# Optimization experiments

Hardware: AMD Instinct MI355X
Metric: run time of the kernel (lower is better)

## Reference

```python
import jax, jax.numpy as jnp
import numpy as np

B, L, HID = 8, 1025, 1024
H, KV, DH = 16, 4, 64
EPS = 1e-6
ROPE_BASE = 10000.0


def _rms_norm(x, w):
    var = jnp.mean(jnp.square(x), axis=-1, keepdims=True)
    return x * jax.lax.rsqrt(var + EPS) * w


def _rotate_half(x):
    x1, x2 = jnp.split(x, 2, axis=-1)
    return jnp.concatenate([-x2, x1], axis=-1)


def _rope_cache(seq_len, dim):
    inv_freq = 1.0 / (ROPE_BASE ** (jnp.arange(0, dim, 2, dtype=jnp.float32) / dim))
    pos = jnp.arange(seq_len, dtype=jnp.float32)
    freqs = pos[:, None] * inv_freq[None, :]            # [L_img, dim/2]
    emb = jnp.concatenate([freqs, freqs], axis=-1)       # [L_img, dim]
    return jnp.cos(emb), jnp.sin(emb)


def setup_inputs() -> dict:
    key = jax.random.key(0)
    ks = jax.random.split(key, 5)
    s_in = 1.0
    s_q = float(np.sqrt(2.0 / (HID + H * DH)))
    s_kv = float(np.sqrt(2.0 / (HID + KV * DH)))
    s_o = float(np.sqrt(2.0 / (H * DH + HID)) / np.sqrt(2.0))
    return {
        "inputs": jax.random.normal(ks[0], (B, L, HID), jnp.float32) * s_in,
        "Wq": jax.random.normal(ks[1], (H * DH, HID), jnp.float32) * s_q,
        "Wk": jax.random.normal(ks[2], (KV * DH, HID), jnp.float32) * s_kv,
        "Wv": jax.random.normal(ks[3], (KV * DH, HID), jnp.float32) * s_kv,
        "Wo": jax.random.normal(ks[4], (HID, H * DH), jnp.float32) * s_o,
        "q_norm_w": jnp.ones((DH,), jnp.float32),
        "k_norm_w": jnp.ones((DH,), jnp.float32),
    }


def reference(inputs, Wq, Wk, Wv, Wo, q_norm_w, k_norm_w):
    b, l, _ = inputs.shape
    # projections (torch Linear: x @ W.T), reshape to heads, QK RMSNorm
    q = (inputs @ Wq.T).reshape(b, l, H, DH)
    k = (inputs @ Wk.T).reshape(b, l, KV, DH)
    v = (inputs @ Wv.T).reshape(b, l, KV, DH)
    q = _rms_norm(q, q_norm_w).transpose(0, 2, 1, 3)    # [B,H,L,DH]
    k = _rms_norm(k, k_norm_w).transpose(0, 2, 1, 3)    # [B,KV,L,DH]
    v = v.transpose(0, 2, 1, 3)                          # [B,KV,L,DH]

    # RoPE only on image tokens (skip first action token)
    l_img = l - 1
    cos, sin = _rope_cache(l_img, DH)                    # [L_img, DH]
    cos = cos[None, None].astype(q.dtype)
    sin = sin[None, None].astype(q.dtype)
    q_img = q[:, :, 1:]
    k_img = k[:, :, 1:]
    q = jnp.concatenate([q[:, :, :1], q_img * cos + _rotate_half(q_img) * sin], axis=2)
    k = jnp.concatenate([k[:, :, :1], k_img * cos + _rotate_half(k_img) * sin], axis=2)

    # GQA: repeat kv heads
    rep = H // KV
    k = jnp.repeat(k, rep, axis=1)                       # [B,H,L,DH]
    v = jnp.repeat(v, rep, axis=1)

    # manual attention: NOTE no 1/sqrt(DH) scaling (faithful to source)
    scores = jnp.einsum("bhqd,bhkd->bhqk", q, k)
    attn = jax.nn.softmax(scores.astype(jnp.float32), axis=-1).astype(q.dtype)
    out = jnp.einsum("bhqk,bhkd->bhqd", attn, v)         # [B,H,L,DH]
    out = out.transpose(0, 2, 1, 3).reshape(b, l, H * DH)
    return out @ Wo.T
```

## Files before the change

kernel.cpp:

```cpp
#include <hip/hip_runtime.h>
#include <hip/hip_bf16.h>

using bf16 = __hip_bfloat16;
typedef __bf16 bf16x8 __attribute__((ext_vector_type(8)));
typedef float f32x4 __attribute__((ext_vector_type(4)));
typedef short short8 __attribute__((ext_vector_type(8)));
typedef unsigned short ushort4v __attribute__((ext_vector_type(4)));

#define MFMA16(a, b, c) __builtin_amdgcn_mfma_f32_16x16x32_bf16((a), (b), (c), 0, 0, 0)

constexpr int B_ = 8, L_ = 1025, H_ = 16, KV_ = 4;
constexpr int LKP_ = 1088;
constexpr int M_ = B_ * L_;

constexpr int NX = 8396800, NWQ = 1048576, NWK = 262144, NWV = 262144,
              NWO = 1048576, NNW = 64;

__device__ __forceinline__ void gl_lds16(const bf16* g, bf16* l) {
  __builtin_amdgcn_global_load_lds(
      (const __attribute__((address_space(1))) void*)g,
      (__attribute__((address_space(3))) void*)l, 16, 0, 0);
}

template <int NWG>
__device__ __forceinline__ int xcd_swz(int orig) {
  constexpr int q = NWG >> 3, r = NWG & 7;
  const int x = orig & 7, idx = orig >> 3;
  return (x < r ? x * (q + 1) : r * (q + 1) + (x - r) * q) + idx;
}

__global__ __launch_bounds__(64) void detect_dtype(const unsigned short* qw_raw,
                                                   int* flag) {
  if (threadIdx.x == 0) flag[0] = (qw_raw[0] == 0x3F80) ? 0 : 1;
}

__global__ __launch_bounds__(256) void convert_all(
    const void* s0, const void* s1, const void* s2, const void* s3,
    const void* s4, const void* s5, const void* s6,
    bf16* d0, bf16* d1, bf16* d2, bf16* d3, bf16* d4, bf16* d5, bf16* d6,
    const int* flag) {
  const int f = *flag;
  const int tid = blockIdx.x * blockDim.x + threadIdx.x;
  const int stride = gridDim.x * blockDim.x;
  auto conv = [&](const void* s, bf16* d, int n) {
    const int n8 = n >> 3;
    if (f) {
      const f32x4* sf = (const f32x4*)s;
      short8* dd = (short8*)d;
      for (int i = tid; i < n8; i += stride) {
        const f32x4 v0 = sf[2 * i], v1 = sf[2 * i + 1];
        short8 o;
#pragma unroll
        for (int j = 0; j < 4; ++j) {
          o[j]     = __builtin_bit_cast(short, __float2bfloat16(v0[j]));
          o[j + 4] = __builtin_bit_cast(short, __float2bfloat16(v1[j]));
        }
        dd[i] = o;
      }
    } else {
      const short8* su = (const short8*)s;
      short8* dd = (short8*)d;
      for (int i = tid; i < n8; i += stride) dd[i] = su[i];
    }
  };
  conv(s0, d0, NX);
  conv(s1, d1, NWQ);
  conv(s2, d2, NWK);
  conv(s3, d3, NWV);
  conv(s4, d4, NWO);
  conv(s5, d5, NNW);
  conv(s6, d6, NNW);
}

__global__ __launch_bounds__(256) void zero_pads(bf16* Kb, bf16* VT) {
  const int idx = blockIdx.x * 256 + threadIdx.x;
  const bf16 z = __float2bfloat16(0.f);
  {
    const int g = idx / 4032, rem = idx % 4032;
    const int r = rem >> 6, d = rem & 63;
    Kb[((size_t)g * LKP_ + 1025 + r) * 64 + d] = z;
  }
  {
    const int row = idx / 63, c = idx % 63;
    VT[(size_t)row * LKP_ + 1025 + c] = z;
  }
}

template <int EPI, int NT, int NWG>
__global__ __launch_bounds__(256) void gemm_bt(
    const bf16* __restrict__ X, const bf16* __restrict__ W0,
    const bf16* __restrict__ W1, const bf16* __restrict__ W2,
    void* __restrict__ O0, bf16* __restrict__ O1, bf16* __restrict__ O2,
    const bf16* __restrict__ qw, const bf16* __restrict__ kw,
    const int* flag) {
  const int wg = xcd_swz<NWG>(blockIdx.x);
  const int m0 = (wg / NT) * 128;
  const int n0 = (wg % NT) * 128;

  int outf32 = 0;
  if constexpr (EPI == 0) outf32 = *flag;

  const bf16* W;
  int nw0;
  if constexpr (EPI == 0) {
    W = W0; nw0 = n0;
  } else {
    if (n0 < 1024)      { W = W0; nw0 = n0; }
    else if (n0 < 1280) { W = W1; nw0 = n0 - 1024; }
    else                { W = W2; nw0 = n0 - 1280; }
  }

  __shared__ bf16 As[128 * 64];
  __shared__ bf16 Bs[128 * 64];

  const int tid = threadIdx.x;
  const int lane = tid & 63, wid = tid >> 6;
  const int wr = wid >> 1, wc = wid & 1;
  const int lo = lane & 15, g = lane >> 4;

  const f32x4 zero4 = {0.f, 0.f, 0.f, 0.f};
  f32x4 acc[4][4];
#pragma unroll
  for (int i = 0; i < 4; ++i)
#pragma unroll
    for (int j = 0; j < 4; ++j) acc[i][j] = zero4;

  const int rr = tid >> 3;
  const int csw = ((tid & 7) ^ (rr & 7)) * 8;
  const bf16* xp[4];
  const bf16* wp[4];
#pragma unroll
  for (int is = 0; is < 4; ++is) {
    int rx = m0 + rr + 32 * is;
    if (rx > M_ - 1) rx = M_ - 1;
    xp[is] = X + (size_t)rx * 1024 + csw;
    wp[is] = W + (size_t)(nw0 + rr + 32 * is) * 1024 + csw;
  }

  for (int kt = 0; kt < 16; ++kt) {
#pragma unroll
    for (int is = 0; is < 4; ++is) {
      gl_lds16(xp[is], &As[is * 2048 + (size_t)tid * 8]);
      gl_lds16(wp[is], &Bs[is * 2048 + (size_t)tid * 8]);
      xp[is] += 64; wp[is] += 64;
    }
    __syncthreads();

    bf16x8 a[2][4], bb[2][4];
#pragma unroll
    for (int kk = 0; kk < 2; ++kk) {
      const int sw = ((4 * kk + g) ^ (lo & 7)) * 8;
#pragma unroll
      for (int i = 0; i < 4; ++i)
        a[kk][i] = *reinterpret_cast<const bf16x8*>(&As[(wr * 64 + i * 16 + lo) * 64 + sw]);
#pragma unroll
      for (int j = 0; j < 4; ++j)
        bb[kk][j] = *reinterpret_cast<const bf16x8*>(&Bs[(wc * 64 + j * 16 + lo) * 64 + sw]);
    }
#pragma unroll
    for (int kk = 0; kk < 2; ++kk)
#pragma unroll
      for (int i = 0; i < 4; ++i)
#pragma unroll
        for (int j = 0; j < 4; ++j)
          acc[i][j] = MFMA16(a[kk][i], bb[kk][j], acc[i][j]);
    __syncthreads();
  }

  const bool qkreg = (EPI == 1) && (n0 < 1280);
  float wv[4];
  float invf0 = 0.f, invf1 = 0.f;
  if (qkreg) {
    const bf16* w = (n0 < 1024) ? qw : kw;
#pragma unroll
    for (int j = 0; j < 4; ++j) wv[j] = __bfloat162float(w[j * 16 + lo]);
    constexpr float c = -0.41524101186092029f;
    invf0 = exp2f((float)lo * c);
    invf1 = invf0 * exp2f(16.f * c);
  }

#pragma unroll
  for (int i = 0; i < 4; ++i) {
#pragma unroll
    for (int ii = 0; ii < 4; ++ii) {
      const int m = m0 + wr * 64 + i * 16 + g * 4 + ii;
      if (m >= M_) continue;
      const int b = m / L_;
      const int l = m % L_;
      float fv[4];
#pragma unroll
      for (int j = 0; j < 4; ++j) fv[j] = acc[i][j][ii];

      if (qkreg) {
#pragma unroll
        for (int j = 0; j < 4; ++j)
          fv[j] = __bfloat162float(__float2bfloat16(fv[j]));
        float ss = fv[0] * fv[0] + fv[1] * fv[1] + fv[2] * fv[2] + fv[3] * fv[3];
        ss += __shfl_xor(ss, 1);
        ss += __shfl_xor(ss, 2);
        ss += __shfl_xor(ss, 4);
        ss += __shfl_xor(ss, 8);
        const float r = rsqrtf(ss * (1.f / 64.f) + 1e-6f);
#pragma unroll
        for (int j = 0; j < 4; ++j) fv[j] *= r * wv[j];
        if (l > 0) {
          const float pos = (float)(l - 1);
          float sn0, cs0, sn1, cs1;
          __sincosf(pos * invf0, &sn0, &cs0);
          __sincosf(pos * invf1, &sn1, &cs1);
          const float a0 = fv[0], a2 = fv[2];
          fv[0] = a0 * cs0 - a2 * sn0;
          fv[2] = a2 * cs0 + a0 * sn0;
          const float a1 = fv[1], a3 = fv[3];
          fv[1] = a1 * cs1 - a3 * sn1;
          fv[3] = a3 * cs1 + a1 * sn1;
        }
      }

#pragma unroll
      for (int j = 0; j < 4; ++j) {
        const int n = n0 + wc * 64 + j * 16 + lo;
        const float f = fv[j];
        if constexpr (EPI == 0) {
          if (outf32) ((float*)O0)[(size_t)m * 1024 + n] = f;
          else        ((bf16*)O0)[(size_t)m * 1024 + n] = __float2bfloat16(f);
        } else {
          const bf16 v = __float2bfloat16(f);
          if (n < 1024) {
            ((bf16*)O0)[((size_t)(b * H_ + (n >> 6)) * L_ + l) * 64 + (n & 63)] = v;
          } else if (n < 1280) {
            const int c2 = n - 1024;
            O1[((size_t)(b * KV_ + (c2 >> 6)) * LKP_ + l) * 64 + (c2 & 63)] = v;
          } else {
            const int c2 = n - 1280;
            O2[((size_t)(b * KV_ + (c2 >> 6)) * 64 + (c2 & 63)) * LKP_ + l] = v;
          }
        }
      }
    }
  }
}

__global__ __launch_bounds__(512) void attn(
    const bf16* __restrict__ Q, const bf16* __restrict__ Kt,
    const bf16* __restrict__ VT, bf16* __restrict__ AO) {
  const int tid = threadIdx.x, lane = tid & 63, w = tid >> 6;
  const int lo = lane & 15, g = lane >> 4;
  const int qt = blockIdx.x, h = blockIdx.y, b = blockIdx.z;
  const int kv = h >> 2;

  __shared__ unsigned short Ks[64 * 64];
  __shared__ unsigned short Vs[64 * 64];
  __shared__ unsigned short Ps[8 * 16 * 64];

  const bf16* qbase = Q + (size_t)(b * H_ + h) * L_ * 64;
  int qrow = qt * 128 + w * 16 + lo;
  if (qrow > L_ - 1) qrow = L_ - 1;
  const bf16x8 qf0 = *reinterpret_cast<const bf16x8*>(qbase + (size_t)qrow * 64 + g * 8);
  const bf16x8 qf1 = *reinterpret_cast<const bf16x8*>(qbase + (size_t)qrow * 64 + 32 + g * 8);

  const f32x4 zero4 = {0.f, 0.f, 0.f, 0.f};
  f32x4 o[4];
  float mi = -3e38f, li = 0.f;
#pragma unroll
  for (int i = 0; i < 4; ++i) o[i] = zero4;

  const int sr = tid >> 3;
  const int scol = (tid & 7) * 8;
  const int swcol = ((tid & 7) ^ (sr & 7)) * 8;
  const bf16* kbase = Kt + ((size_t)(b * KV_ + kv) * LKP_ + sr) * 64 + scol;
  const bf16* vbase = VT + ((size_t)(b * KV_ + kv) * 64 + sr) * LKP_ + scol;

  const int sw0 = (g ^ (lo & 7)) * 8;
  const int sw1 = ((4 | g) ^ (lo & 7)) * 8;
  const int pswa = ((g >> 1) ^ (lo & 7));

  for (int kt = 0; kt < 17; ++kt) {
    const int k0 = kt * 64;
    const short8 ka = *reinterpret_cast<const short8*>(kbase + (size_t)k0 * 64);
    const short8 va = *reinterpret_cast<const short8*>(vbase + k0);
    __syncthreads();
    *reinterpret_cast<short8*>(&Ks[sr * 64 + swcol]) = ka;
    *reinterpret_cast<short8*>(&Vs[sr * 64 + swcol]) = va;
    __syncthreads();

    f32x4 s[4];
#pragma unroll
    for (int kb = 0; kb < 4; ++kb) {
      f32x4 t = zero4;
      const bf16x8 ka0 = *reinterpret_cast<const bf16x8*>(&Ks[(kb * 16 + lo) * 64 + sw0]);
      const bf16x8 ka1 = *reinterpret_cast<const bf16x8*>(&Ks[(kb * 16 + lo) * 64 + sw1]);
      t = MFMA16(ka0, qf0, t);
      t = MFMA16(ka1, qf1, t);
      s[kb] = t;
    }
    if (kt == 16) {
#pragma unroll
      for (int kb = 0; kb < 4; ++kb)
#pragma unroll
        for (int i = 0; i < 4; ++i)
          if (k0 + kb * 16 + g * 4 + i >= L_) s[kb][i] = -1e30f;
    }

    float t0 = fmaxf(fmaxf(s[0][0], s[0][1]), fmaxf(s[0][2], s[0][3]));
    float t1 = fmaxf(fmaxf(s[1][0], s[1][1]), fmaxf(s[1][2], s[1][3]));
    float t2 = fmaxf(fmaxf(s[2][0], s[2][1]), fmaxf(s[2][2], s[2][3]));
    float t3 = fmaxf(fmaxf(s[3][0], s[3][1]), fmaxf(s[3][2], s[3][3]));
    float tm = fmaxf(fmaxf(t0, t1), fmaxf(t2, t3));
    tm = fmaxf(tm, __shfl_xor(tm, 16));
    tm = fmaxf(tm, __shfl_xor(tm, 32));
    if (!__all(tm <= mi)) {
      const float mn = fmaxf(mi, tm);
      const float sc = __expf(mi - mn);
      mi = mn;
      li *= sc;
#pragma unroll
      for (int db = 0; db < 4; ++db)
#pragma unroll
        for (int i = 0; i < 4; ++i) o[db][i] *= sc;
    }
#pragma unroll
    for (int kb = 0; kb < 4; ++kb)
#pragma unroll
      for (int i = 0; i < 4; ++i) s[kb][i] = __expf(s[kb][i] - mi);
    float p0 = (s[0][0] + s[0][1]) + (s[0][2] + s[0][3]);
    float p1 = (s[1][0] + s[1][1]) + (s[1][2] + s[1][3]);
    float p2 = (s[2][0] + s[2][1]) + (s[2][2] + s[2][3]);
    float p3 = (s[3][0] + s[3][1]) + (s[3][2] + s[3][3]);
    float ps = (p0 + p1) + (p2 + p3);
    ps += __shfl_xor(ps, 16);
    ps += __shfl_xor(ps, 32);
    li += ps;

#pragma unroll
    for (int kb = 0; kb < 4; ++kb) {
      ushort4v pk;
#pragma unroll
      for (int i = 0; i < 4; ++i)
        pk[i] = __builtin_bit_cast(unsigned short, __float2bfloat16(s[kb][i]));
      *reinterpret_cast<ushort4v*>(
          &Ps[w * 1024 + lo * 64 + ((2 * kb) ^ pswa ^ (g >> 1) ^ (g >> 1)) * 8 +
              (((2 * kb + (g >> 1)) ^ (lo & 7)) - ((2 * kb) ^ pswa ^ (g >> 1) ^ (g >> 1))) * 8 +
              (g & 1) * 4]) = pk;
    }

    const bf16x8 pb0 = *reinterpret_cast<const bf16x8*>(&Ps[w * 1024 + lo * 64 + sw0]);
    const bf16x8 pb1 = *reinterpret_cast<const bf16x8*>(&Ps[w * 1024 + lo * 64 + sw1]);
#pragma unroll
    for (int db = 0; db < 4; ++db) {
      const bf16x8 va0 = *reinterpret_cast<const bf16x8*>(&Vs[(db * 16 + lo) * 64 + sw0]);
      const bf16x8 va1 = *reinterpret_cast<const bf16x8*>(&Vs[(db * 16 + lo) * 64 + sw1]);
      o[db] = MFMA16(va0, pb0, o[db]);
      o[db] = MFMA16(va1, pb1, o[db]);
    }
  }

  const int qr = qt * 128 + w * 16 + lo;
  if (qr < L_) {
    const float inv = 1.f / li;
    unsigned* base = (unsigned*)(AO + ((size_t)b * L_ + qr) * 1024 + h * 64);
#pragma unroll
    for (int db = 0; db < 4; ++db) {
#pragma unroll
      for (int i2 = 0; i2 < 4; i2 += 2) {
        const unsigned u0 = __builtin_bit_cast(unsigned short,
                                __float2bfloat16(o[db][i2] * inv));
        const unsigned u1 = __builtin_bit_cast(unsigned short,
                                __float2bfloat16(o[db][i2 + 1] * inv));
        base[(db * 16 + 4 * g + i2) >> 1] = u0 | (u1 << 16);
      }
    }
  }
}

extern "C" void kernel_launch(void* const* d_in, const int* in_sizes, int n_in,
                              void* d_out, int out_size, void* d_ws, size_t ws_size,
                              hipStream_t stream) {
  (void)in_sizes; (void)n_in; (void)out_size; (void)ws_size;

  char* wsb = (char*)d_ws;
  int* flagp = (int*)wsb;
  bf16* cX  = (bf16*)(wsb + 16);
  bf16* cWq = cX + NX;
  bf16* cWk = cWq + NWQ;
  bf16* cWv = cWk + NWK;
  bf16* cWo = cWv + NWV;
  bf16* cqw = cWo + NWO;
  bf16* ckw = cqw + NNW;
  bf16* Qb  = ckw + NNW;
  bf16* Kb  = Qb  + (size_t)B_ * H_ * L_ * 64;
  bf16* VTb = Kb  + (size_t)B_ * KV_ * LKP_ * 64;
  bf16* AOb = VTb + (size_t)B_ * KV_ * 64 * LKP_;

  detect_dtype<<<1, 64, 0, stream>>>((const unsigned short*)d_in[5], flagp);
  convert_all<<<2048, 256, 0, stream>>>(
      d_in[0], d_in[1], d_in[2], d_in[3], d_in[4], d_in[5], d_in[6],
      cX, cWq, cWk, cWv, cWo, cqw, ckw, flagp);
  zero_pads<<<504, 256, 0, stream>>>(Kb, VTb);

  gemm_bt<1, 12, 780><<<780, 256, 0, stream>>>(cX, cWq, cWk, cWv, Qb, Kb, VTb,
                                               cqw, ckw, nullptr);
  attn<<<dim3(9, 16, 8), 512, 0, stream>>>(Qb, Kb, VTb, AOb);
  gemm_bt<0, 8, 520><<<520, 256, 0, stream>>>(AOb, cWo, nullptr, nullptr, d_out,
                                              nullptr, nullptr, nullptr, nullptr,
                                              flagp);
}
```

Measured before the change: 212.8 us.

## Double-buffer GEMM LDS tiles and prefetch K/V tiles in attention loop

The projection GEMM now uses two 128x32 LDS buffers per operand with a K-step of 32. The next tile's global-to-LDS loads are issued before computing on the current one, so load latency can overlap the MFMAs. The attention kernel loads the next K/V tile into registers right after the LDS store, brackets its MFMA sections with s_setprio, and simplifies the P swizzle index math. The cost is twice as many loop iterations with fewer MFMAs per barrier, plus extra register pressure from the prefetched K/V values.

```diff
diff --git a/kernel.cpp b/kernel.cpp
--- a/kernel.cpp
+++ b/kernel.cpp
@@ -110,8 +110,8 @@
     else                { W = W2; nw0 = n0 - 1280; }
   }
 
-  __shared__ bf16 As[128 * 64];
-  __shared__ bf16 Bs[128 * 64];
+  __shared__ bf16 As[2][128 * 32];
+  __shared__ bf16 Bs[2][128 * 32];
 
   const int tid = threadIdx.x;
   const int lane = tid & 63, wid = tid >> 6;
@@ -125,45 +125,44 @@
 #pragma unroll
     for (int j = 0; j < 4; ++j) acc[i][j] = zero4;
 
-  const int rr = tid >> 3;
-  const int csw = ((tid & 7) ^ (rr & 7)) * 8;
-  const bf16* xp[4];
-  const bf16* wp[4];
-#pragma unroll
-  for (int is = 0; is < 4; ++is) {
-    int rx = m0 + rr + 32 * is;
-    if (rx > M_ - 1) rx = M_ - 1;
-    xp[is] = X + (size_t)rx * 1024 + csw;
-    wp[is] = W + (size_t)(nw0 + rr + 32 * is) * 1024 + csw;
-  }
-
-  for (int kt = 0; kt < 16; ++kt) {
-#pragma unroll
-    for (int is = 0; is < 4; ++is) {
-      gl_lds16(xp[is], &As[is * 2048 + (size_t)tid * 8]);
-      gl_lds16(wp[is], &Bs[is * 2048 + (size_t)tid * 8]);
-      xp[is] += 64; wp[is] += 64;
-    }
-    __syncthreads();
-
-    bf16x8 a[2][4], bb[2][4];
-#pragma unroll
-    for (int kk = 0; kk < 2; ++kk) {
-      const int sw = ((4 * kk + g) ^ (lo & 7)) * 8;
-#pragma unroll
-      for (int i = 0; i < 4; ++i)
-        a[kk][i] = *reinterpret_cast<const bf16x8*>(&As[(wr * 64 + i * 16 + lo) * 64 + sw]);
+  const int rr = tid >> 2;
+  const int csw = ((tid & 3) ^ ((rr >> 1) & 3)) * 8;
+  int xr0 = m0 + rr;      if (xr0 > M_ - 1) xr0 = M_ - 1;
+  int xr1 = m0 + 64 + rr; if (xr1 > M_ - 1) xr1 = M_ - 1;
+  const bf16* xp0 = X + (size_t)xr0 * 1024 + csw;
+  const bf16* xp1 = X + (size_t)xr1 * 1024 + csw;
+  const bf16* wp0 = W + (size_t)(nw0 + rr) * 1024 + csw;
+  const bf16* wp1 = W + (size_t)(nw0 + 64 + rr) * 1024 + csw;
+
+  auto stage = [&](int buf) {
+    gl_lds16(xp0, &As[buf][(size_t)tid * 8]);
+    gl_lds16(xp1, &As[buf][2048 + (size_t)tid * 8]);
+    gl_lds16(wp0, &Bs[buf][(size_t)tid * 8]);
+    gl_lds16(wp1, &Bs[buf][2048 + (size_t)tid * 8]);
+    xp0 += 32; xp1 += 32; wp0 += 32; wp1 += 32;
+  };
+
+  stage(0);
+  __syncthreads();
+
+  const int swl = (g ^ ((lo >> 1) & 3)) * 8;
+
+  for (int kt = 0; kt < 32; ++kt) {
+    const int cur = kt & 1;
+    if (kt < 31) stage(cur ^ 1);
+
+    bf16x8 a[4], bb[4];
+#pragma unroll
+    for (int i = 0; i < 4; ++i)
+      a[i] = *reinterpret_cast<const bf16x8*>(&As[cur][(wr * 64 + i * 16 + lo) * 32 + swl]);
+#pragma unroll
+    for (int j = 0; j < 4; ++j)
+      bb[j] = *reinterpret_cast<const bf16x8*>(&Bs[cur][(wc * 64 + j * 16 + lo) * 32 + swl]);
+#pragma unroll
+    for (int i = 0; i < 4; ++i)
 #pragma unroll
       for (int j = 0; j < 4; ++j)
-        bb[kk][j] = *reinterpret_cast<const bf16x8*>(&Bs[(wc * 64 + j * 16 + lo) * 64 + sw]);
-    }
-#pragma unroll
-    for (int kk = 0; kk < 2; ++kk)
-#pragma unroll
-      for (int i = 0; i < 4; ++i)
-#pragma unroll
-        for (int j = 0; j < 4; ++j)
-          acc[i][j] = MFMA16(a[kk][i], bb[kk][j], acc[i][j]);
+        acc[i][j] = MFMA16(a[i], bb[j], acc[i][j]);
     __syncthreads();
   }
 
@@ -268,23 +267,30 @@
   const int sr = tid >> 3;
   const int scol = (tid & 7) * 8;
   const int swcol = ((tid & 7) ^ (sr & 7)) * 8;
-  const bf16* kbase = Kt + ((size_t)(b * KV_ + kv) * LKP_ + sr) * 64 + scol;
-  const bf16* vbase = VT + ((size_t)(b * KV_ + kv) * 64 + sr) * LKP_ + scol;
+  const bf16* kptr = Kt + ((size_t)(b * KV_ + kv) * LKP_ + sr) * 64 + scol;
+  const bf16* vptr = VT + ((size_t)(b * KV_ + kv) * 64 + sr) * LKP_ + scol;
 
   const int sw0 = (g ^ (lo & 7)) * 8;
   const int sw1 = ((4 | g) ^ (lo & 7)) * 8;
-  const int pswa = ((g >> 1) ^ (lo & 7));
+
+  short8 ka = *reinterpret_cast<const short8*>(kptr);
+  short8 va = *reinterpret_cast<const short8*>(vptr);
 
   for (int kt = 0; kt < 17; ++kt) {
-    const int k0 = kt * 64;
-    const short8 ka = *reinterpret_cast<const short8*>(kbase + (size_t)k0 * 64);
-    const short8 va = *reinterpret_cast<const short8*>(vbase + k0);
     __syncthreads();
     *reinterpret_cast<short8*>(&Ks[sr * 64 + swcol]) = ka;
     *reinterpret_cast<short8*>(&Vs[sr * 64 + swcol]) = va;
     __syncthreads();
 
+    if (kt < 16) {
+      kptr += 64 * 64;
+      vptr += 64;
+      ka = *reinterpret_cast<const short8*>(kptr);
+      va = *reinterpret_cast<const short8*>(vptr);
+    }
+
     f32x4 s[4];
+    __builtin_amdgcn_s_setprio(1);
 #pragma unroll
     for (int kb = 0; kb < 4; ++kb) {
       f32x4 t = zero4;
@@ -294,12 +300,13 @@
       t = MFMA16(ka1, qf1, t);
       s[kb] = t;
     }
+    __builtin_amdgcn_s_setprio(0);
     if (kt == 16) {
 #pragma unroll
       for (int kb = 0; kb < 4; ++kb)
 #pragma unroll
         for (int i = 0; i < 4; ++i)
-          if (k0 + kb * 16 + g * 4 + i >= L_) s[kb][i] = -1e30f;
+          if (kt * 64 + kb * 16 + g * 4 + i >= L_) s[kb][i] = -1e30f;
     }
 
     float t0 = fmaxf(fmaxf(s[0][0], s[0][1]), fmaxf(s[0][2], s[0][3]));
@@ -338,14 +345,13 @@
 #pragma unroll
       for (int i = 0; i < 4; ++i)
         pk[i] = __builtin_bit_cast(unsigned short, __float2bfloat16(s[kb][i]));
-      *reinterpret_cast<ushort4v*>(
-          &Ps[w * 1024 + lo * 64 + ((2 * kb) ^ pswa ^ (g >> 1) ^ (g >> 1)) * 8 +
-              (((2 * kb + (g >> 1)) ^ (lo & 7)) - ((2 * kb) ^ pswa ^ (g >> 1) ^ (g >> 1))) * 8 +
-              (g & 1) * 4]) = pk;
+      const int pblk = (2 * kb + (g >> 1)) ^ (lo & 7);
+      *reinterpret_cast<ushort4v*>(&Ps[w * 1024 + lo * 64 + pblk * 8 + (g & 1) * 4]) = pk;
     }
 
     const bf16x8 pb0 = *reinterpret_cast<const bf16x8*>(&Ps[w * 1024 + lo * 64 + sw0]);
     const bf16x8 pb1 = *reinterpret_cast<const bf16x8*>(&Ps[w * 1024 + lo * 64 + sw1]);
+    __builtin_amdgcn_s_setprio(1);
 #pragma unroll
     for (int db = 0; db < 4; ++db) {
       const bf16x8 va0 = *reinterpret_cast<const bf16x8*>(&Vs[(db * 16 + lo) * 64 + sw0]);
@@ -353,6 +359,7 @@
       o[db] = MFMA16(va0, pb0, o[db]);
       o[db] = MFMA16(va1, pb1, o[db]);
     }
+    __builtin_amdgcn_s_setprio(0);
   }
 
   const int qr = qt * 128 + w * 16 + lo;
```

After: 227.8 us. +7.0%, slower.
